# Performance work log

Measured on AMD Instinct MI355X. Metric: run time of the kernel, lower is better.

Reference implementation:

```python
import jax, jax.numpy as jnp
import numpy as np

N_NODES = 100000


def gcn_conv(x, src, dst, W, b, num_nodes):
    # PyG GCNConv: add self-loops, symmetric normalization D^-1/2 (A+I) D^-1/2, then linear.
    loop = jnp.arange(num_nodes, dtype=src.dtype)
    s = jnp.concatenate([src, loop])
    d = jnp.concatenate([dst, loop])
    deg = jax.ops.segment_sum(jnp.ones_like(d, dtype=x.dtype), d, num_segments=num_nodes)
    dinv = jnp.where(deg > 0, jax.lax.rsqrt(deg), 0.0)
    norm = dinv[s] * dinv[d]                       # [E+N]
    h = x @ W                                      # [N, out]
    msg = h[s] * norm[:, None]                     # gather + scale
    out = jax.ops.segment_sum(msg, d, num_segments=num_nodes)  # scatter-add
    return out + b


def setup_inputs() -> dict:
    key = jax.random.key(0)
    k1, k2, k3, k4 = jax.random.split(key, 4)
    F_IN, HID, C = 165, 128, 2
    E = 3200000
    x = jax.random.normal(k1, (N_NODES, F_IN), dtype=jnp.float32)
    edge_index = jax.random.randint(k2, (2, E), 0, N_NODES, dtype=jnp.int64)
    W1 = jax.random.normal(k3, (F_IN, HID), dtype=jnp.float32) * (1.0 / np.sqrt(F_IN))
    b1 = jnp.zeros((HID,), dtype=jnp.float32)
    W2 = jax.random.normal(k4, (HID, C), dtype=jnp.float32) * (1.0 / np.sqrt(HID))
    b2 = jnp.zeros((C,), dtype=jnp.float32)
    return {"x": x, "edge_index": edge_index, "W1": W1, "b1": b1, "W2": W2, "b2": b2}


def reference(x, edge_index, W1, b1, W2, b2):
    src, dst = edge_index[0], edge_index[1]
    h = jax.nn.relu(gcn_conv(x, src, dst, W1, b1, N_NODES))
    # dropout is identity in eval mode (self.training=False)
    out = gcn_conv(h, src, dst, W2, b2, N_NODES)
    return out
```

## Files before the change

### kernel.cpp

```cpp
#include <hip/hip_runtime.h>

#define NN  100000
#define FIN 165
#define HID 128
#define NBUCK 391
#define CHUNK 8192
#define CAP   9216
#define KPAD 192
#define XS 36

typedef __attribute__((ext_vector_type(4))) float f32x4;
typedef __attribute__((ext_vector_type(8))) short short8;

#define OFF_DINV   0
#define OFF_H1     100352
#define OFF_Z      (OFF_H1 + NN * 64)
#define OFF_ROWPTR (OFF_Z + 2 * NN)
#define OFF_GBASE  (OFF_ROWPTR + 100352)
#define OFF_GCUR   (OFF_GBASE + 512)
#define OFF_BUCK   (OFF_GCUR + 512)
#define OFF_EDATA  (OFF_BUCK + NBUCK * CAP)
#define OFF_WTHI   (OFF_EDATA + 3200000)

__device__ __forceinline__ unsigned bf16rne(float f) {
    unsigned u = __float_as_uint(f);
    return (u + 0x7FFFu + ((u >> 16) & 1u)) >> 16;
}

__device__ __forceinline__ float2 bf2_to_f2(unsigned int u) {
    float2 r;
    r.x = __uint_as_float(u << 16);
    r.y = __uint_as_float(u & 0xffff0000u);
    return r;
}

__device__ __forceinline__ short8 ldfrag(const ushort* p) {
    union { uint2 u[2]; short8 s; } f;
    f.u[0] = *(const uint2*)p;
    f.u[1] = *(const uint2*)(p + 16);
    return f.s;
}

__global__ void k_wsplit(const float* __restrict__ W1, ushort* __restrict__ hi,
                         int* __restrict__ gcur) {
    int t = blockIdx.x * blockDim.x + threadIdx.x;
    if (t < 512) gcur[t] = t * CAP;
    if (t >= HID * KPAD) return;
    int ch = t / KPAD, k = t % KPAD;
    float v = (k < FIN) ? W1[k * HID + ch] : 0.0f;
    hi[ch * KPAD + k] = (ushort)bf16rne(v);
}

__global__ __launch_bounds__(256) void k_bfill(const int* __restrict__ src,
        const int* __restrict__ dst, int* __restrict__ gcur,
        unsigned int* __restrict__ bucketed, int ne) {
    __shared__ int hist[NBUCK];
    __shared__ int lcur[NBUCK];
    for (int i = threadIdx.x; i < NBUCK; i += 256) hist[i] = 0;
    __syncthreads();
    const int4* dst4 = (const int4*)dst;
    const int4* src4 = (const int4*)src;
    const int ne4 = ne >> 2;
    const int base4 = blockIdx.x * (CHUNK / 4);
#pragma unroll
    for (int it = 0; it < CHUNK / 1024; ++it) {
        int e4 = base4 + it * 256 + threadIdx.x;
        if (e4 < ne4) {
            int4 v = dst4[e4];
            atomicAdd(&hist[v.x >> 8], 1);
            atomicAdd(&hist[v.y >> 8], 1);
            atomicAdd(&hist[v.z >> 8], 1);
            atomicAdd(&hist[v.w >> 8], 1);
        }
    }
    if (blockIdx.x == 0 && threadIdx.x < (ne & 3))
        atomicAdd(&hist[dst[(ne & ~3) + threadIdx.x] >> 8], 1);
    __syncthreads();
    for (int i = threadIdx.x; i < NBUCK; i += 256) {
        int h = hist[i];
        lcur[i] = h ? atomicAdd(&gcur[i], h) : 0;
    }
    __syncthreads();
#define PUT(D, S)                                                            \
    {                                                                        \
        int b_ = (D) >> 8;                                                   \
        int pos_ = atomicAdd(&lcur[b_], 1);                                  \
        if (pos_ < (b_ + 1) * CAP)                                           \
            bucketed[pos_] = (unsigned)(S) | ((unsigned)((D) & 255) << 24);  \
    }
#pragma unroll
    for (int it = 0; it < CHUNK / 1024; ++it) {
        int e4 = base4 + it * 256 + threadIdx.x;
        if (e4 < ne4) {
            int4 d4 = dst4[e4];
            int4 s4 = src4[e4];
            PUT(d4.x, s4.x);
            PUT(d4.y, s4.y);
            PUT(d4.z, s4.z);
            PUT(d4.w, s4.w);
        }
    }
    if (blockIdx.x == 0 && threadIdx.x < (ne & 3)) {
        int e = (ne & ~3) + threadIdx.x;
        PUT(dst[e], src[e]);
    }
#undef PUT
}

__global__ __launch_bounds__(512) void k_bscan(const int* __restrict__ gcur,
        int* __restrict__ gbase) {
    __shared__ int s[512];
    int tid = threadIdx.x;
    int c = 0;
    if (tid < NBUCK) {
        c = gcur[tid] - tid * CAP;
        c = min(c, CAP);
    }
    s[tid] = c;
    __syncthreads();
    for (int off = 1; off < 512; off <<= 1) {
        int t = (tid >= off) ? s[tid - off] : 0;
        __syncthreads();
        s[tid] += t;
        __syncthreads();
    }
    if (tid < NBUCK) gbase[tid] = s[tid] - c;
    if (tid == NBUCK - 1) gbase[NBUCK] = s[tid];
}

__global__ __launch_bounds__(256) void k_fine(const int* __restrict__ gbase,
        const unsigned int* __restrict__ bucketed, int* __restrict__ edata,
        int* __restrict__ rowptr, float* __restrict__ dinv, int n) {
    __shared__ int hist[256];
    __shared__ int scan[256];
    __shared__ int lcur[256];
    const int b = blockIdx.x;
    const int tid = threadIdx.x;
    const int rbeg = b * CAP;
    const int wbeg = gbase[b], wend = gbase[b + 1];
    const int cnt = wend - wbeg;
    hist[tid] = 0;
    __syncthreads();
    for (int j = tid; j < cnt; j += 256)
        atomicAdd(&hist[bucketed[rbeg + j] >> 24], 1);
    __syncthreads();
    int c = hist[tid];
    scan[tid] = c;
    __syncthreads();
    for (int off = 1; off < 256; off <<= 1) {
        int t = (tid >= off) ? scan[tid - off] : 0;
        __syncthreads();
        scan[tid] += t;
        __syncthreads();
    }
    int excl = scan[tid] - c;
    int d = b * 256 + tid;
    if (d < n) {
        rowptr[d] = wbeg + excl;
        dinv[d] = rsqrtf((float)c + 1.0f);
    }
    lcur[tid] = wbeg + excl;
    __syncthreads();
    for (int j = tid; j < cnt; j += 256) {
        unsigned p = bucketed[rbeg + j];
        int pos = atomicAdd(&lcur[p >> 24], 1);
        edata[pos] = (int)(p & 0x00FFFFFFu);
    }
    if (b == NBUCK - 1 && tid == 0) rowptr[n] = wend;
}

__global__ __launch_bounds__(256) void k_gemm1(const float* __restrict__ x,
        const ushort* __restrict__ wthi, unsigned* __restrict__ h1, int n) {
    __shared__ alignas(16) ushort xhi[64 * XS];
    __shared__ alignas(16) ushort whi[128 * XS];
    const int tid = threadIdx.x;
    const int node0 = blockIdx.x * 64;
    const int wv = tid >> 6, lane = tid & 63;
    const int r15 = lane & 15, g = lane >> 4;
    f32x4 acc[8];
#pragma unroll
    for (int ct = 0; ct < 8; ++ct) acc[ct] = (f32x4){0.f, 0.f, 0.f, 0.f};

    const int snd = tid >> 2, sq = tid & 3;
    const int sch = tid >> 1, sh = tid & 1;

    for (int ks = 0; ks < 6; ++ks) {
        {
            int gidx = sch * KPAD + ks * 32 + sh * 16;
            int lidx = sch * XS + sh * 16;
            uint4 a = *(const uint4*)&wthi[gidx];
            uint4 b = *(const uint4*)&wthi[gidx + 8];
            *(uint2*)&whi[lidx]      = make_uint2(a.x, a.y);
            *(uint2*)&whi[lidx + 4]  = make_uint2(a.z, a.w);
            *(uint2*)&whi[lidx + 8]  = make_uint2(b.x, b.y);
            *(uint2*)&whi[lidx + 12] = make_uint2(b.z, b.w);
        }
        {
            int node = node0 + snd;
            unsigned h8[8];
#pragma unroll
            for (int j = 0; j < 8; ++j) {
                int kk = ks * 32 + sq * 8 + j;
                float v = (node < n && kk < FIN) ? x[node * FIN + kk] : 0.0f;
                h8[j] = bf16rne(v);
            }
            int lidx = snd * XS + sq * 8;
            *(uint2*)&xhi[lidx]     = make_uint2(h8[0] | (h8[1] << 16), h8[2] | (h8[3] << 16));
            *(uint2*)&xhi[lidx + 4] = make_uint2(h8[4] | (h8[5] << 16), h8[6] | (h8[7] << 16));
        }
        __syncthreads();
        short8 Ah = ldfrag(&xhi[(wv * 16 + r15) * XS + 4 * g]);
#pragma unroll
        for (int ct = 0; ct < 8; ++ct) {
            short8 Bh = ldfrag(&whi[(ct * 16 + r15) * XS + 4 * g]);
            acc[ct] = __builtin_amdgcn_mfma_f32_16x16x32_bf16(Ah, Bh, acc[ct], 0, 0, 0);
        }
        __syncthreads();
    }
#pragma unroll
    for (int ct = 0; ct < 4; ++ct) {
#pragma unroll
        for (int r = 0; r < 4; ++r) {
            int node = node0 + wv * 16 + 4 * g + r;
            if (node < n) {
                unsigned p = bf16rne(acc[ct][r]) | (bf16rne(acc[ct + 4][r]) << 16);
                h1[node * 64 + ct * 16 + r15] = p;
            }
        }
    }
}

__global__ __launch_bounds__(256) void k_agg_fused(const int* __restrict__ rowptr,
        const int* __restrict__ edata, const unsigned int* __restrict__ h1,
        const float* __restrict__ dinv, const float* __restrict__ b1,
        const float* __restrict__ W2, float* __restrict__ z, int n0, int nn) {
    const int wid  = (blockIdx.x * blockDim.x + threadIdx.x) >> 6;
    const int lane = threadIdx.x & 63;
    if (wid >= nn) return;
    const int d = n0 + wid;
    const int beg = rowptr[d], end = rowptr[d + 1];
    const float di = dinv[d];
    const int grp = lane >> 4;
    const int sl  = lane & 15;

    float ax0, ax1, ax2, ax3, ay0, ay1, ay2, ay3;
    {
        uint4 hv = *(const uint4*)&h1[d * 64 + sl * 4];
        float nm = (grp == 0) ? di * di : 0.0f;
        float2 f0 = bf2_to_f2(hv.x), f1 = bf2_to_f2(hv.y);
        float2 f2 = bf2_to_f2(hv.z), f3 = bf2_to_f2(hv.w);
        ax0 = f0.x * nm; ay0 = f0.y * nm;
        ax1 = f1.x * nm; ay1 = f1.y * nm;
        ax2 = f2.x * nm; ay2 = f2.y * nm;
        ax3 = f3.x * nm; ay3 = f3.y * nm;
    }

#define PRELOAD(JB)                                                          \
    {                                                                        \
        int i0 = (JB) + grp, i1 = (JB) + 4 + grp,                            \
            i2 = (JB) + 8 + grp, i3 = (JB) + 12 + grp;                       \
        int c0 = min(i0, end - 1), c1 = min(i1, end - 1);                    \
        int c2 = min(i2, end - 1), c3 = min(i3, end - 1);                    \
        s0 = edata[c0]; s1 = edata[c1]; s2 = edata[c2]; s3 = edata[c3];      \
        m0 = (i0 < end) ? dinv[s0] * di : 0.0f;                              \
        m1 = (i1 < end) ? dinv[s1] * di : 0.0f;                              \
        m2 = (i2 < end) ? dinv[s2] * di : 0.0f;                              \
        m3 = (i3 < end) ? dinv[s3] * di : 0.0f;                              \
    }
#define ACC(G, NM)                                                           \
    {                                                                        \
        float2 f;                                                            \
        f = bf2_to_f2((G).x); ax0 = fmaf(f.x, (NM), ax0); ay0 = fmaf(f.y, (NM), ay0); \
        f = bf2_to_f2((G).y); ax1 = fmaf(f.x, (NM), ax1); ay1 = fmaf(f.y, (NM), ay1); \
        f = bf2_to_f2((G).z); ax2 = fmaf(f.x, (NM), ax2); ay2 = fmaf(f.y, (NM), ay2); \
        f = bf2_to_f2((G).w); ax3 = fmaf(f.x, (NM), ax3); ay3 = fmaf(f.y, (NM), ay3); \
    }

    if (beg < end) {
        int s0, s1, s2, s3;
        float m0, m1, m2, m3;
        PRELOAD(beg);
        for (int j = beg; j < end; j += 16) {
            uint4 g0 = *(const uint4*)&h1[s0 * 64 + sl * 4];
            uint4 g1 = *(const uint4*)&h1[s1 * 64 + sl * 4];
            uint4 g2 = *(const uint4*)&h1[s2 * 64 + sl * 4];
            uint4 g3 = *(const uint4*)&h1[s3 * 64 + sl * 4];
            float w0 = m0, w1 = m1, w2 = m2, w3 = m3;
            int jn = j + 16;
            if (jn < end) PRELOAD(jn);
            ACC(g0, w0); ACC(g1, w1); ACC(g2, w2); ACC(g3, w3);
        }
    }
#undef PRELOAD
#undef ACC

    ax0 += __shfl_xor(ax0, 16, 64); ax0 += __shfl_xor(ax0, 32, 64);
    ax1 += __shfl_xor(ax1, 16, 64); ax1 += __shfl_xor(ax1, 32, 64);
    ax2 += __shfl_xor(ax2, 16, 64); ax2 += __shfl_xor(ax2, 32, 64);
    ax3 += __shfl_xor(ax3, 16, 64); ax3 += __shfl_xor(ax3, 32, 64);
    ay0 += __shfl_xor(ay0, 16, 64); ay0 += __shfl_xor(ay0, 32, 64);
    ay1 += __shfl_xor(ay1, 16, 64); ay1 += __shfl_xor(ay1, 32, 64);
    ay2 += __shfl_xor(ay2, 16, 64); ay2 += __shfl_xor(ay2, 32, 64);
    ay3 += __shfl_xor(ay3, 16, 64); ay3 += __shfl_xor(ay3, 32, 64);
    const int c = sl * 4;
    float4 bA = *(const float4*)&b1[c];
    float4 bB = *(const float4*)&b1[c + 64];
    float v00 = ax0 + bA.x; v00 = v00 > 0.f ? v00 : 0.f;
    float v01 = ax1 + bA.y; v01 = v01 > 0.f ? v01 : 0.f;
    float v02 = ax2 + bA.z; v02 = v02 > 0.f ? v02 : 0.f;
    float v03 = ax3 + bA.w; v03 = v03 > 0.f ? v03 : 0.f;
    float v10 = ay0 + bB.x; v10 = v10 > 0.f ? v10 : 0.f;
    float v11 = ay1 + bB.y; v11 = v11 > 0.f ? v11 : 0.f;
    float v12 = ay2 + bB.z; v12 = v12 > 0.f ? v12 : 0.f;
    float v13 = ay3 + bB.w; v13 = v13 > 0.f ? v13 : 0.f;
    float4 wA0 = *(const float4*)&W2[c * 2];
    float4 wA1 = *(const float4*)&W2[c * 2 + 4];
    float4 wB0 = *(const float4*)&W2[(c + 64) * 2];
    float4 wB1 = *(const float4*)&W2[(c + 64) * 2 + 4];
    float p0 = v00 * wA0.x + v01 * wA0.z + v02 * wA1.x + v03 * wA1.z
             + v10 * wB0.x + v11 * wB0.z + v12 * wB1.x + v13 * wB1.z;
    float p1 = v00 * wA0.y + v01 * wA0.w + v02 * wA1.y + v03 * wA1.w
             + v10 * wB0.y + v11 * wB0.w + v12 * wB1.y + v13 * wB1.w;
#pragma unroll
    for (int m = 8; m >= 1; m >>= 1) {
        p0 += __shfl_xor(p0, m, 64);
        p1 += __shfl_xor(p1, m, 64);
    }
    if (lane == 0) *(float2*)&z[d * 2] = make_float2(p0, p1);
}

__global__ __launch_bounds__(256) void k_out(const int* __restrict__ rowptr,
        const int* __restrict__ edata, const float* __restrict__ z,
        const float* __restrict__ dinv, const float* __restrict__ b2,
        float* __restrict__ out, int n) {
    int g = (blockIdx.x * blockDim.x + threadIdx.x) >> 4;
    int l = threadIdx.x & 15;
    if (g >= n) return;
    int beg = rowptr[g], end = rowptr[g + 1];
    float di = dinv[g];
    float o0 = 0.0f, o1 = 0.0f;
    for (int j = beg + l; j < end; j += 16) {
        int s = edata[j];
        float nm = dinv[s] * di;
        float2 zs = *(const float2*)&z[s * 2];
        o0 = fmaf(zs.x, nm, o0);
        o1 = fmaf(zs.y, nm, o1);
    }
#pragma unroll
    for (int m = 8; m >= 1; m >>= 1) {
        o0 += __shfl_xor(o0, m, 16);
        o1 += __shfl_xor(o1, m, 16);
    }
    if (l == 0) {
        float2 zd = *(const float2*)&z[g * 2];
        float s2 = di * di;
        out[g * 2]     = fmaf(zd.x, s2, b2[0]) + o0;
        out[g * 2 + 1] = fmaf(zd.y, s2, b2[1]) + o1;
    }
}

extern "C" void kernel_launch(void* const* d_in, const int* in_sizes, int n_in,
                              void* d_out, int out_size, void* d_ws, size_t ws_size,
                              hipStream_t stream) {
    const float* x  = (const float*)d_in[0];
    const int*   ei = (const int*)d_in[1];
    const float* W1 = (const float*)d_in[2];
    const float* b1 = (const float*)d_in[3];
    const float* W2 = (const float*)d_in[4];
    const float* b2 = (const float*)d_in[5];
    float* out = (float*)d_out;

    const int n  = in_sizes[0] / FIN;
    const int ne = in_sizes[1] / 2;
    const int* src = ei;
    const int* dst = ei + ne;

    float* ws     = (float*)d_ws;
    float* dinv   = ws + OFF_DINV;
    unsigned int* h1 = (unsigned int*)(ws + OFF_H1);
    float* z      = ws + OFF_Z;
    int*   rowptr = (int*)(ws + OFF_ROWPTR);
    int*   gbase  = (int*)(ws + OFF_GBASE);
    int*   gcur   = (int*)(ws + OFF_GCUR);
    unsigned int* bucketed = (unsigned int*)(ws + OFF_BUCK);
    int*   edata  = (int*)(ws + OFF_EDATA);
    ushort* wthi  = (ushort*)(ws + OFF_WTHI);

    const int nchb = (ne + CHUNK - 1) / CHUNK;

    k_wsplit<<<(HID * KPAD + 255) / 256, 256, 0, stream>>>(W1, wthi, gcur);
    k_bfill<<<nchb, 256, 0, stream>>>(src, dst, gcur, bucketed, ne);
    k_bscan<<<1, 512, 0, stream>>>(gcur, gbase);
    k_fine<<<NBUCK, 256, 0, stream>>>(gbase, bucketed, edata, rowptr, dinv, n);
    k_gemm1<<<(n + 63) / 64, 256, 0, stream>>>(x, wthi, h1, n);
    const int q = (n + 3) / 4;
    for (int i = 0; i < 4; ++i) {
        int n0 = i * q;
        int nn = (n - n0 < q) ? (n - n0) : q;
        if (nn > 0)
            k_agg_fused<<<((size_t)nn * 64 + 255) / 256, 256, 0, stream>>>(
                rowptr, edata, h1, dinv, b1, W2, z, n0, nn);
    }
    k_out<<<(n * 16 + 255) / 256, 256, 0, stream>>>(rowptr, edata, z, dinv, b2, out, n);
}
```

Measured before the change: 266.5 us.

## Preload full W tile into LDS once and load x fragments directly to registers

The first-layer GEMM kernel now copies the entire padded bf16 weight matrix into shared memory once per block and drops the per-k-step staging of both W and x. Each lane loads its own x row elements straight from global memory, converts them to bf16 and packs the MFMA A fragment in registers. This removes two barriers per k-step and the LDS round trip for x. In exchange it uses more LDS, which may lower occupancy, and the per-lane x loads are strided across rows rather than coalesced.

```diff
diff --git a/kernel.cpp b/kernel.cpp
--- a/kernel.cpp
+++ b/kernel.cpp
@@ -7,7 +7,7 @@
 #define CHUNK 8192
 #define CAP   9216
 #define KPAD 192
-#define XS 36
+#define WS   196
 
 typedef __attribute__((ext_vector_type(4))) float f32x4;
 typedef __attribute__((ext_vector_type(8))) short short8;
@@ -171,52 +171,56 @@
 
 __global__ __launch_bounds__(256) void k_gemm1(const float* __restrict__ x,
         const ushort* __restrict__ wthi, unsigned* __restrict__ h1, int n) {
-    __shared__ alignas(16) ushort xhi[64 * XS];
-    __shared__ alignas(16) ushort whi[128 * XS];
+    __shared__ alignas(16) ushort whi[128 * WS];
     const int tid = threadIdx.x;
     const int node0 = blockIdx.x * 64;
     const int wv = tid >> 6, lane = tid & 63;
     const int r15 = lane & 15, g = lane >> 4;
+
+    {
+        int ch = tid >> 1, h = tid & 1;
+        int gb = ch * KPAD + h * 96;
+        int lb = ch * WS + h * 96;
+#pragma unroll
+        for (int j = 0; j < 24; ++j) {
+            uint2 v = *(const uint2*)&wthi[gb + j * 4];
+            *(uint2*)&whi[lb + j * 4] = v;
+        }
+    }
+
     f32x4 acc[8];
 #pragma unroll
     for (int ct = 0; ct < 8; ++ct) acc[ct] = (f32x4){0.f, 0.f, 0.f, 0.f};
 
-    const int snd = tid >> 2, sq = tid & 3;
-    const int sch = tid >> 1, sh = tid & 1;
+    const int row = node0 + wv * 16 + r15;
+    const bool rowok = row < n;
+    const float* xrow = x + (size_t)row * FIN;
+
+    __syncthreads();
 
     for (int ks = 0; ks < 6; ++ks) {
-        {
-            int gidx = sch * KPAD + ks * 32 + sh * 16;
-            int lidx = sch * XS + sh * 16;
-            uint4 a = *(const uint4*)&wthi[gidx];
-            uint4 b = *(const uint4*)&wthi[gidx + 8];
-            *(uint2*)&whi[lidx]      = make_uint2(a.x, a.y);
-            *(uint2*)&whi[lidx + 4]  = make_uint2(a.z, a.w);
-            *(uint2*)&whi[lidx + 8]  = make_uint2(b.x, b.y);
-            *(uint2*)&whi[lidx + 12] = make_uint2(b.z, b.w);
-        }
-        {
-            int node = node0 + snd;
-            unsigned h8[8];
-#pragma unroll
-            for (int j = 0; j < 8; ++j) {
-                int kk = ks * 32 + sq * 8 + j;
-                float v = (node < n && kk < FIN) ? x[node * FIN + kk] : 0.0f;
-                h8[j] = bf16rne(v);
-            }
-            int lidx = snd * XS + sq * 8;
-            *(uint2*)&xhi[lidx]     = make_uint2(h8[0] | (h8[1] << 16), h8[2] | (h8[3] << 16));
-            *(uint2*)&xhi[lidx + 4] = make_uint2(h8[4] | (h8[5] << 16), h8[6] | (h8[7] << 16));
-        }
-        __syncthreads();
-        short8 Ah = ldfrag(&xhi[(wv * 16 + r15) * XS + 4 * g]);
+        unsigned hh[8];
+#pragma unroll
+        for (int j = 0; j < 4; ++j) {
+            int k0 = ks * 32 + 4 * g + j;
+            int k1 = k0 + 16;
+            float v0 = (rowok && k0 < FIN) ? xrow[k0] : 0.0f;
+            float v1 = (rowok && k1 < FIN) ? xrow[k1] : 0.0f;
+            hh[j]     = bf16rne(v0);
+            hh[4 + j] = bf16rne(v1);
+        }
+        union { unsigned u[4]; short8 s; } A;
+        A.u[0] = hh[0] | (hh[1] << 16);
+        A.u[1] = hh[2] | (hh[3] << 16);
+        A.u[2] = hh[4] | (hh[5] << 16);
+        A.u[3] = hh[6] | (hh[7] << 16);
 #pragma unroll
         for (int ct = 0; ct < 8; ++ct) {
-            short8 Bh = ldfrag(&whi[(ct * 16 + r15) * XS + 4 * g]);
-            acc[ct] = __builtin_amdgcn_mfma_f32_16x16x32_bf16(Ah, Bh, acc[ct], 0, 0, 0);
-        }
-        __syncthreads();
-    }
+            short8 Bh = ldfrag(&whi[(ct * 16 + r15) * WS + ks * 32 + 4 * g]);
+            acc[ct] = __builtin_amdgcn_mfma_f32_16x16x32_bf16(A.s, Bh, acc[ct], 0, 0, 0);
+        }
+    }
+
 #pragma unroll
     for (int ct = 0; ct < 4; ++ct) {
 #pragma unroll
```

New measurement: 263.7 us. About the same (-1.0%).
